# Performance work log

Measured on AMD Instinct MI355X. Metric: run time of the kernel, lower is better.

## Reference

```python
import jax, jax.numpy as jnp
import numpy as np

HID = 8
PRED_LEN = 12
SCALE = 4.4


def lstm_cell(x, h, c, Wih, Whh, bih, bhh):
    # torch.nn.LSTMCell gate order: i, f, g, o
    gates = x @ Wih.T + h @ Whh.T + (bih + bhh)  # (B, 4*HID)
    i, f, g, o = jnp.split(gates, 4, axis=-1)
    i = jax.nn.sigmoid(i)
    f = jax.nn.sigmoid(f)
    g = jnp.tanh(g)
    o = jax.nn.sigmoid(o)
    c_new = f * c + i * g
    h_new = o * jnp.tanh(c_new)
    return h_new, c_new


def setup_inputs() -> dict:
    key = jax.random.key(0)
    ks = jax.random.split(key, 12)
    B = 1048576
    obs_traj = jax.random.normal(ks[0], (8, B, 2), dtype=jnp.float32)
    h0 = jax.random.normal(ks[1], (B, HID), dtype=jnp.float32)
    c0 = jax.random.normal(ks[2], (B, HID), dtype=jnp.float32)
    s = 0.1
    Wih_t = jax.random.normal(ks[3], (4 * HID, 2), dtype=jnp.float32) * s
    Whh_t = jax.random.normal(ks[4], (4 * HID, HID), dtype=jnp.float32) * s
    bih_t = jax.random.normal(ks[5], (4 * HID,), dtype=jnp.float32) * s
    bhh_t = jax.random.normal(ks[6], (4 * HID,), dtype=jnp.float32) * s
    Wih_p = jax.random.normal(ks[7], (4 * HID, 2), dtype=jnp.float32) * s
    Whh_p = jax.random.normal(ks[8], (4 * HID, HID), dtype=jnp.float32) * s
    bih_p = jax.random.normal(ks[9], (4 * HID,), dtype=jnp.float32) * s
    bhh_p = jax.random.normal(ks[10], (4 * HID,), dtype=jnp.float32) * s
    Wp = jax.random.normal(ks[11], (2, HID), dtype=jnp.float32) * s
    bp = jnp.zeros((2,), dtype=jnp.float32)
    return {"obs_traj": obs_traj, "h0": h0, "c0": c0,
            "Wih_t": Wih_t, "Whh_t": Whh_t, "bih_t": bih_t, "bhh_t": bhh_t,
            "Wih_p": Wih_p, "Whh_p": Whh_p, "bih_p": bih_p, "bhh_p": bhh_p,
            "Wp": Wp, "bp": bp}


def reference(obs_traj, h0, c0, Wih_t, Whh_t, bih_t, bhh_t,
              Wih_p, Whh_p, bih_p, bhh_p, Wp, bp):
    B = obs_traj.shape[1]

    # --- encoder: scan over obs_len steps ---
    def enc_step(carry, x_t):
        h, c = carry
        x = jax.nn.relu(x_t)  # F.relu(input_t)
        h, c = lstm_cell(x, h, c, Wih_t, Whh_t, bih_t, bhh_t)
        return (h, c), None

    (h_enc, _), _ = jax.lax.scan(enc_step, (h0, c0), obs_traj)

    h_dec = h_enc
    c_dec = jnp.zeros_like(h_enc)
    out0 = jnp.zeros((B, 2), dtype=obs_traj.dtype)

    def dec_step(carry, _):
        h, c, out = carry
        x = jax.lax.stop_gradient(out)  # output.detach()
        h, c = lstm_cell(x, h, c, Wih_p, Whh_p, bih_p, bhh_p)
        out = jnp.tanh(h @ Wp.T + bp) * SCALE
        return (h, c, out), out

    _, pred_traj = jax.lax.scan(dec_step, (h_dec, c_dec, out0), None, length=PRED_LEN)
    return pred_traj  # (PRED_LEN, B, 2)
```

## Files before the change

kernel.cpp:

```cpp
#include <hip/hip_runtime.h>

#define HID 8
#define OBS_LEN 8
#define PRED_LEN 12
#define SCALE 4.4f
#define BLOCK 256
#define ELEMS_PER_BLOCK 128

typedef __attribute__((ext_vector_type(8)))  _Float16 half8;
typedef __attribute__((ext_vector_type(16))) float    f32x16;

#define LOG2E 1.44269504f

struct AB { half8 hi, lo; };
struct H2 { _Float16 hi, lo; };

__device__ __forceinline__ H2 split1(float v) {
    H2 r;
    r.hi = (_Float16)v;
    r.lo = (_Float16)(v - (float)r.hi);
    return r;
}

__device__ __forceinline__ void inv_pair(float a, float b, float& ia, float& ib) {
    const float r = __builtin_amdgcn_rcpf(a * b);
    ia = r * b;
    ib = r * a;
}

__device__ __forceinline__ AB build_A(int m, int half,
    const float* __restrict__ Wih, const float* __restrict__ Whh,
    const float* __restrict__ bih, const float* __restrict__ bhh)
{
    float w[8];
    if (half == 0) {
        w[0] = Wih[m * 2 + 0];
        w[1] = Wih[m * 2 + 1];
        w[2] = Whh[m * 8 + 0];
        w[3] = Whh[m * 8 + 1];
        w[4] = Whh[m * 8 + 2];
        w[5] = Whh[m * 8 + 3];
        w[6] = bih[m] + bhh[m];
        w[7] = 0.0f;
    } else {
        w[0] = 0.0f;
        w[1] = 0.0f;
        w[2] = Whh[m * 8 + 4];
        w[3] = Whh[m * 8 + 5];
        w[4] = Whh[m * 8 + 6];
        w[5] = Whh[m * 8 + 7];
        w[6] = 0.0f;
        w[7] = 0.0f;
    }
    AB r;
#pragma unroll
    for (int i = 0; i < 8; ++i) {
        const H2 s = split1(w[i]);
        r.hi[i] = s.hi;
        r.lo[i] = s.lo;
    }
    return r;
}

__device__ __forceinline__ AB build_B(float x0, float x1, const float h[4]) {
    AB r;
    const float v[6] = { x0, x1, h[0], h[1], h[2], h[3] };
#pragma unroll
    for (int i = 0; i < 6; ++i) {
        const H2 s = split1(v[i]);
        r.hi[i] = s.hi;
        r.lo[i] = s.lo;
    }
    r.hi[6] = (_Float16)1.0f; r.lo[6] = (_Float16)0.0f;
    r.hi[7] = (_Float16)0.0f; r.lo[7] = (_Float16)0.0f;
    return r;
}

__device__ __forceinline__ void lstm_pointwise(const f32x16& acc, float c[4], float h[4]) {
    float num1[4], den1[4], uo[4];
#pragma unroll
    for (int j = 0; j < 4; ++j) {
        const float ai = acc[j], af = acc[4 + j], ag = acc[8 + j], ao = acc[12 + j];
        const float ei = __builtin_amdgcn_exp2f(ai * -LOG2E);
        const float ef = __builtin_amdgcn_exp2f(af * -LOG2E);
        const float eg = __builtin_amdgcn_exp2f(ag * (-2.0f * LOG2E));
        const float eo = __builtin_amdgcn_exp2f(ao * -LOG2E);
        const float ui = 1.0f + ei, uf = 1.0f + ef, vg = 1.0f + eg;
        const float tg = 1.0f - eg;
        const float uiv = ui * vg;
        num1[j] = fmaf(tg, uf, c[j] * uiv);
        den1[j] = uf * uiv;
        uo[j] = 1.0f + eo;
    }
    float inv1[4];
    inv_pair(den1[0], den1[1], inv1[0], inv1[1]);
    inv_pair(den1[2], den1[3], inv1[2], inv1[3]);

    float den2[4], tc[4];
#pragma unroll
    for (int j = 0; j < 4; ++j) {
        const float cn = num1[j] * inv1[j];
        c[j] = cn;
        const float s = fminf(cn * (-2.0f * LOG2E), 43.0f);
        const float ec = __builtin_amdgcn_exp2f(s);
        den2[j] = uo[j] * (1.0f + ec);
        tc[j] = 1.0f - ec;
    }
    float inv2[4];
    inv_pair(den2[0], den2[1], inv2[0], inv2[1]);
    inv_pair(den2[2], den2[3], inv2[2], inv2[3]);
#pragma unroll
    for (int j = 0; j < 4; ++j) h[j] = tc[j] * inv2[j];
}

__device__ __forceinline__ void lstm_mfma_step(const AB& A, const AB& B,
                                               float c[4], float h[4]) {
    f32x16 acc = {};
    acc = __builtin_amdgcn_mfma_f32_32x32x16_f16(A.hi, B.hi, acc, 0, 0, 0);
    acc = __builtin_amdgcn_mfma_f32_32x32x16_f16(A.hi, B.lo, acc, 0, 0, 0);
    acc = __builtin_amdgcn_mfma_f32_32x32x16_f16(A.lo, B.hi, acc, 0, 0, 0);
    lstm_pointwise(acc, c, h);
}

__global__ __launch_bounds__(BLOCK) void MYLSTM_88201448390683_kernel(
    const float* __restrict__ obs,
    const float* __restrict__ h0,
    const float* __restrict__ c0,
    const float* __restrict__ Wih_t, const float* __restrict__ Whh_t,
    const float* __restrict__ bih_t, const float* __restrict__ bhh_t,
    const float* __restrict__ Wih_p, const float* __restrict__ Whh_p,
    const float* __restrict__ bih_p, const float* __restrict__ bhh_p,
    const float* __restrict__ Wp,
    const float* __restrict__ bp,
    float* __restrict__ out,
    int B)
{
    const int lane = threadIdx.x & 63;
    const int wid  = threadIdx.x >> 6;
    const int e    = lane & 31;
    const int half = lane >> 5;

    int eg = blockIdx.x * ELEMS_PER_BLOCK + wid * 32 + e;
    const bool ok = eg < B;
    if (!ok) eg = 0;

    float h[4], c[4];
    {
        const float4 hv = *reinterpret_cast<const float4*>(h0 + (size_t)eg * HID + half * 4);
        const float4 cv = *reinterpret_cast<const float4*>(c0 + (size_t)eg * HID + half * 4);
        h[0] = hv.x; h[1] = hv.y; h[2] = hv.z; h[3] = hv.w;
        c[0] = cv.x; c[1] = cv.y; c[2] = cv.z; c[3] = cv.w;
    }

    {
        const AB Aenc = build_A(e, half, Wih_t, Whh_t, bih_t, bhh_t);
#pragma unroll 1
        for (int t = 0; t < OBS_LEN; ++t) {
            const float2 xv = *reinterpret_cast<const float2*>(obs + ((size_t)t * B + eg) * 2);
            const AB Bv = build_B(fmaxf(xv.x, 0.0f), fmaxf(xv.y, 0.0f), h);
            lstm_mfma_step(Aenc, Bv, c, h);
        }
    }

    const AB Adec = build_A(e, half, Wih_p, Whh_p, bih_p, bhh_p);
#pragma unroll
    for (int j = 0; j < 4; ++j) c[j] = 0.0f;

    float wa[4], wb[4];
#pragma unroll
    for (int j = 0; j < 4; ++j) {
        wa[j] = Wp[4 * half + j];
        wb[j] = Wp[HID + 4 * half + j];
    }
    const float bp0 = bp[0], bp1 = bp[1];

    float x0 = 0.0f, x1 = 0.0f;
#pragma unroll 1
    for (int t = 0; t < PRED_LEN; ++t) {
        const AB Bv = build_B(x0, x1, h);
        lstm_mfma_step(Adec, Bv, c, h);
        float a0 = wa[0] * h[0] + wa[1] * h[1] + wa[2] * h[2] + wa[3] * h[3];
        float a1 = wb[0] * h[0] + wb[1] * h[1] + wb[2] * h[2] + wb[3] * h[3];
        a0 += __shfl_xor(a0, 32);
        a1 += __shfl_xor(a1, 32);
        a0 += bp0; a1 += bp1;
        const float e0 = __builtin_amdgcn_exp2f(a0 * (-2.0f * LOG2E));
        const float e1 = __builtin_amdgcn_exp2f(a1 * (-2.0f * LOG2E));
        float i0, i1;
        inv_pair(1.0f + e0, 1.0f + e1, i0, i1);
        x0 = (1.0f - e0) * i0 * SCALE;
        x1 = (1.0f - e1) * i1 * SCALE;
        if (!half && ok) {
            *reinterpret_cast<float2*>(out + ((size_t)t * B + eg) * 2) = make_float2(x0, x1);
        }
    }
}

extern "C" void kernel_launch(void* const* d_in, const int* in_sizes, int n_in,
                              void* d_out, int out_size, void* d_ws, size_t ws_size,
                              hipStream_t stream) {
    const float* obs   = (const float*)d_in[0];
    const float* h0    = (const float*)d_in[1];
    const float* c0    = (const float*)d_in[2];
    const float* Wih_t = (const float*)d_in[3];
    const float* Whh_t = (const float*)d_in[4];
    const float* bih_t = (const float*)d_in[5];
    const float* bhh_t = (const float*)d_in[6];
    const float* Wih_p = (const float*)d_in[7];
    const float* Whh_p = (const float*)d_in[8];
    const float* bih_p = (const float*)d_in[9];
    const float* bhh_p = (const float*)d_in[10];
    const float* Wp    = (const float*)d_in[11];
    const float* bp    = (const float*)d_in[12];
    float* out = (float*)d_out;

    const int B = in_sizes[1] / HID;
    const int grid = (B + ELEMS_PER_BLOCK - 1) / ELEMS_PER_BLOCK;

    hipLaunchKernelGGL(MYLSTM_88201448390683_kernel, dim3(grid), dim3(BLOCK), 0, stream,
                       obs, h0, c0,
                       Wih_t, Whh_t, bih_t, bhh_t,
                       Wih_p, Whh_p, bih_p, bhh_p,
                       Wp, bp, out, B);
}
```

Before: 367.1 us.

## Fold exp2 scaling into MFMA weights and vectorize LSTM pointwise math as packed float2

Pre-multiplies the gate weights and biases by -log2e (or -2·log2e for the g gate) so the MFMA accumulator feeds exp2 directly, removing per-element multiplies. Rewrites the pointwise math using 2-wide float vectors so the compiler can emit packed FP32 ops, uses cvt_pkrtz for the fp16 hi/lo splits, and merges the four reciprocals per step into a single rcp. Adds a clamp on the g-gate exponent and lowers the tanh(c) clamp. Risks: round-to-zero fp16 conversion, the fourfold product feeding one rcp could overflow or underflow, and the clamps may cause small accuracy differences.

```diff
diff --git a/kernel.cpp b/kernel.cpp
--- a/kernel.cpp
+++ b/kernel.cpp
@@ -7,116 +7,132 @@
 #define BLOCK 256
 #define ELEMS_PER_BLOCK 128
 
+#define LOG2E 1.44269504f
+#define ECLAMP 16.0f
+
 typedef __attribute__((ext_vector_type(8)))  _Float16 half8;
+typedef __attribute__((ext_vector_type(2)))  _Float16 half2v;
 typedef __attribute__((ext_vector_type(16))) float    f32x16;
-
-#define LOG2E 1.44269504f
-
+typedef __attribute__((ext_vector_type(2)))  float    v2f;
+
+union H8 { half8 v; half2v p[4]; };
 struct AB { half8 hi, lo; };
-struct H2 { _Float16 hi, lo; };
-
-__device__ __forceinline__ H2 split1(float v) {
-    H2 r;
-    r.hi = (_Float16)v;
-    r.lo = (_Float16)(v - (float)r.hi);
+
+__device__ __forceinline__ v2f splat(float v) { v2f r; r.x = v; r.y = v; return r; }
+
+__device__ __forceinline__ v2f exp2v(v2f a) {
+    v2f r;
+    r.x = __builtin_amdgcn_exp2f(a.x);
+    r.y = __builtin_amdgcn_exp2f(a.y);
     return r;
 }
 
-__device__ __forceinline__ void inv_pair(float a, float b, float& ia, float& ib) {
-    const float r = __builtin_amdgcn_rcpf(a * b);
-    ia = r * b;
-    ib = r * a;
-}
-
-__device__ __forceinline__ AB build_A(int m, int half,
+__device__ __forceinline__ half2v pkrtz(float a, float b) {
+    return __builtin_bit_cast(half2v, __builtin_amdgcn_cvt_pkrtz(a, b));
+}
+
+__device__ __forceinline__ void split_pair(float a, float b, half2v& hi, half2v& lo) {
+    hi = pkrtz(a, b);
+    lo = pkrtz(a - (float)hi.x, b - (float)hi.y);
+}
+
+__device__ __forceinline__ void quad_inv(const v2f d[2], v2f inv[2]) {
+    const v2f p2 = d[0] * d[1];
+    const float r = __builtin_amdgcn_rcpf(p2.x * p2.y);
+    const v2f t = splat(r) * p2;
+    v2f ts; ts.x = t.y; ts.y = t.x;
+    inv[0] = ts * d[1];
+    inv[1] = ts * d[0];
+}
+
+__device__ __forceinline__ AB build_A(int m, int half_,
     const float* __restrict__ Wih, const float* __restrict__ Whh,
     const float* __restrict__ bih, const float* __restrict__ bhh)
 {
+    const float k = ((m >> 3) == 2) ? (-2.0f * LOG2E) : (-LOG2E);
     float w[8];
-    if (half == 0) {
-        w[0] = Wih[m * 2 + 0];
-        w[1] = Wih[m * 2 + 1];
-        w[2] = Whh[m * 8 + 0];
-        w[3] = Whh[m * 8 + 1];
-        w[4] = Whh[m * 8 + 2];
-        w[5] = Whh[m * 8 + 3];
-        w[6] = bih[m] + bhh[m];
+    if (half_ == 0) {
+        w[0] = Wih[m * 2 + 0] * k;
+        w[1] = Wih[m * 2 + 1] * k;
+        w[2] = Whh[m * 8 + 0] * k;
+        w[3] = Whh[m * 8 + 1] * k;
+        w[4] = Whh[m * 8 + 2] * k;
+        w[5] = Whh[m * 8 + 3] * k;
+        w[6] = (bih[m] + bhh[m]) * k;
         w[7] = 0.0f;
     } else {
         w[0] = 0.0f;
         w[1] = 0.0f;
-        w[2] = Whh[m * 8 + 4];
-        w[3] = Whh[m * 8 + 5];
-        w[4] = Whh[m * 8 + 6];
-        w[5] = Whh[m * 8 + 7];
+        w[2] = Whh[m * 8 + 4] * k;
+        w[3] = Whh[m * 8 + 5] * k;
+        w[4] = Whh[m * 8 + 6] * k;
+        w[5] = Whh[m * 8 + 7] * k;
         w[6] = 0.0f;
         w[7] = 0.0f;
     }
-    AB r;
+    H8 hi, lo;
 #pragma unroll
-    for (int i = 0; i < 8; ++i) {
-        const H2 s = split1(w[i]);
-        r.hi[i] = s.hi;
-        r.lo[i] = s.lo;
-    }
+    for (int i = 0; i < 4; ++i) split_pair(w[2 * i], w[2 * i + 1], hi.p[i], lo.p[i]);
+    AB r; r.hi = hi.v; r.lo = lo.v;
     return r;
 }
 
-__device__ __forceinline__ AB build_B(float x0, float x1, const float h[4]) {
-    AB r;
-    const float v[6] = { x0, x1, h[0], h[1], h[2], h[3] };
+__device__ __forceinline__ AB build_B(float x0, float x1, const v2f h[2]) {
+    H8 hi, lo;
+    split_pair(x0, x1, hi.p[0], lo.p[0]);
+    split_pair(h[0].x, h[0].y, hi.p[1], lo.p[1]);
+    split_pair(h[1].x, h[1].y, hi.p[2], lo.p[2]);
+    const half2v one0 = {(_Float16)1.0f, (_Float16)0.0f};
+    const half2v zz   = {(_Float16)0.0f, (_Float16)0.0f};
+    hi.p[3] = one0;
+    lo.p[3] = zz;
+    AB r; r.hi = hi.v; r.lo = lo.v;
+    return r;
+}
+
+__device__ __forceinline__ void lstm_pointwise(const f32x16& acc, v2f c[2], v2f h[2]) {
+    v2f num1[2], den1[2], uo[2];
 #pragma unroll
-    for (int i = 0; i < 6; ++i) {
-        const H2 s = split1(v[i]);
-        r.hi[i] = s.hi;
-        r.lo[i] = s.lo;
-    }
-    r.hi[6] = (_Float16)1.0f; r.lo[6] = (_Float16)0.0f;
-    r.hi[7] = (_Float16)0.0f; r.lo[7] = (_Float16)0.0f;
-    return r;
-}
-
-__device__ __forceinline__ void lstm_pointwise(const f32x16& acc, float c[4], float h[4]) {
-    float num1[4], den1[4], uo[4];
+    for (int p = 0; p < 2; ++p) {
+        v2f ai, af, agr, ao;
+        ai.x  = acc[2 * p + 0];  ai.y  = acc[2 * p + 1];
+        af.x  = acc[4 + 2 * p];  af.y  = acc[5 + 2 * p];
+        agr.x = acc[8 + 2 * p];  agr.y = acc[9 + 2 * p];
+        ao.x  = acc[12 + 2 * p]; ao.y  = acc[13 + 2 * p];
+        const v2f ag = __builtin_elementwise_min(agr, splat(ECLAMP));
+        const v2f ei = exp2v(ai);
+        const v2f ef = exp2v(af);
+        const v2f eg = exp2v(ag);
+        const v2f eo = exp2v(ao);
+        const v2f ui = 1.0f + ei, uf = 1.0f + ef, vg = 1.0f + eg;
+        const v2f tg = 1.0f - eg;
+        const v2f uiv = ui * vg;
+        num1[p] = tg * uf + c[p] * uiv;
+        den1[p] = uf * uiv;
+        uo[p] = 1.0f + eo;
+    }
+    v2f inv1[2];
+    quad_inv(den1, inv1);
+
+    v2f den2[2], tc[2];
 #pragma unroll
-    for (int j = 0; j < 4; ++j) {
-        const float ai = acc[j], af = acc[4 + j], ag = acc[8 + j], ao = acc[12 + j];
-        const float ei = __builtin_amdgcn_exp2f(ai * -LOG2E);
-        const float ef = __builtin_amdgcn_exp2f(af * -LOG2E);
-        const float eg = __builtin_amdgcn_exp2f(ag * (-2.0f * LOG2E));
-        const float eo = __builtin_amdgcn_exp2f(ao * -LOG2E);
-        const float ui = 1.0f + ei, uf = 1.0f + ef, vg = 1.0f + eg;
-        const float tg = 1.0f - eg;
-        const float uiv = ui * vg;
-        num1[j] = fmaf(tg, uf, c[j] * uiv);
-        den1[j] = uf * uiv;
-        uo[j] = 1.0f + eo;
-    }
-    float inv1[4];
-    inv_pair(den1[0], den1[1], inv1[0], inv1[1]);
-    inv_pair(den1[2], den1[3], inv1[2], inv1[3]);
-
-    float den2[4], tc[4];
-#pragma unroll
-    for (int j = 0; j < 4; ++j) {
-        const float cn = num1[j] * inv1[j];
-        c[j] = cn;
-        const float s = fminf(cn * (-2.0f * LOG2E), 43.0f);
-        const float ec = __builtin_amdgcn_exp2f(s);
-        den2[j] = uo[j] * (1.0f + ec);
-        tc[j] = 1.0f - ec;
-    }
-    float inv2[4];
-    inv_pair(den2[0], den2[1], inv2[0], inv2[1]);
-    inv_pair(den2[2], den2[3], inv2[2], inv2[3]);
-#pragma unroll
-    for (int j = 0; j < 4; ++j) h[j] = tc[j] * inv2[j];
-}
-
-__device__ __forceinline__ void lstm_mfma_step(const AB& A, const AB& B,
-                                               float c[4], float h[4]) {
-    f32x16 acc = {};
-    acc = __builtin_amdgcn_mfma_f32_32x32x16_f16(A.hi, B.hi, acc, 0, 0, 0);
+    for (int p = 0; p < 2; ++p) {
+        const v2f cn = num1[p] * inv1[p];
+        c[p] = cn;
+        const v2f s = __builtin_elementwise_min(cn * (-2.0f * LOG2E), splat(ECLAMP));
+        const v2f ec = exp2v(s);
+        den2[p] = uo[p] * (1.0f + ec);
+        tc[p] = 1.0f - ec;
+    }
+    v2f inv2[2];
+    quad_inv(den2, inv2);
+    h[0] = tc[0] * inv2[0];
+    h[1] = tc[1] * inv2[1];
+}
+
+__device__ __forceinline__ void lstm_mfma_step(const AB& A, const AB& B, const f32x16& Z,
+                                               v2f c[2], v2f h[2]) {
+    f32x16 acc = __builtin_amdgcn_mfma_f32_32x32x16_f16(A.hi, B.hi, Z, 0, 0, 0);
     acc = __builtin_amdgcn_mfma_f32_32x32x16_f16(A.hi, B.lo, acc, 0, 0, 0);
     acc = __builtin_amdgcn_mfma_f32_32x32x16_f16(A.lo, B.hi, acc, 0, 0, 0);
     lstm_pointwise(acc, c, h);
@@ -144,52 +160,56 @@
     const bool ok = eg < B;
     if (!ok) eg = 0;
 
-    float h[4], c[4];
+    const f32x16 kZero = {};
+
+    v2f h[2], c[2];
     {
         const float4 hv = *reinterpret_cast<const float4*>(h0 + (size_t)eg * HID + half * 4);
         const float4 cv = *reinterpret_cast<const float4*>(c0 + (size_t)eg * HID + half * 4);
-        h[0] = hv.x; h[1] = hv.y; h[2] = hv.z; h[3] = hv.w;
-        c[0] = cv.x; c[1] = cv.y; c[2] = cv.z; c[3] = cv.w;
+        h[0].x = hv.x; h[0].y = hv.y; h[1].x = hv.z; h[1].y = hv.w;
+        c[0].x = cv.x; c[0].y = cv.y; c[1].x = cv.z; c[1].y = cv.w;
     }
 
     {
         const AB Aenc = build_A(e, half, Wih_t, Whh_t, bih_t, bhh_t);
 #pragma unroll 1
         for (int t = 0; t < OBS_LEN; ++t) {
-            const float2 xv = *reinterpret_cast<const float2*>(obs + ((size_t)t * B + eg) * 2);
-            const AB Bv = build_B(fmaxf(xv.x, 0.0f), fmaxf(xv.y, 0.0f), h);
-            lstm_mfma_step(Aenc, Bv, c, h);
+            const v2f xv = *reinterpret_cast<const v2f*>(obs + ((size_t)t * B + eg) * 2);
+            const v2f xr = __builtin_elementwise_max(xv, splat(0.0f));
+            const AB Bv = build_B(xr.x, xr.y, h);
+            lstm_mfma_step(Aenc, Bv, kZero, c, h);
         }
     }
 
     const AB Adec = build_A(e, half, Wih_p, Whh_p, bih_p, bhh_p);
-#pragma unroll
-    for (int j = 0; j < 4; ++j) c[j] = 0.0f;
-
-    float wa[4], wb[4];
-#pragma unroll
-    for (int j = 0; j < 4; ++j) {
-        wa[j] = Wp[4 * half + j];
-        wb[j] = Wp[HID + 4 * half + j];
-    }
+    c[0] = splat(0.0f);
+    c[1] = splat(0.0f);
+
+    v2f wa[2], wb[2];
+    wa[0].x = Wp[4 * half + 0];       wa[0].y = Wp[4 * half + 1];
+    wa[1].x = Wp[4 * half + 2];       wa[1].y = Wp[4 * half + 3];
+    wb[0].x = Wp[HID + 4 * half + 0]; wb[0].y = Wp[HID + 4 * half + 1];
+    wb[1].x = Wp[HID + 4 * half + 2]; wb[1].y = Wp[HID + 4 * half + 3];
     const float bp0 = bp[0], bp1 = bp[1];
 
     float x0 = 0.0f, x1 = 0.0f;
 #pragma unroll 1
     for (int t = 0; t < PRED_LEN; ++t) {
         const AB Bv = build_B(x0, x1, h);
-        lstm_mfma_step(Adec, Bv, c, h);
-        float a0 = wa[0] * h[0] + wa[1] * h[1] + wa[2] * h[2] + wa[3] * h[3];
-        float a1 = wb[0] * h[0] + wb[1] * h[1] + wb[2] * h[2] + wb[3] * h[3];
+        lstm_mfma_step(Adec, Bv, kZero, c, h);
+        const v2f q0 = wa[0] * h[0] + wa[1] * h[1];
+        const v2f q1 = wb[0] * h[0] + wb[1] * h[1];
+        float a0 = q0.x + q0.y;
+        float a1 = q1.x + q1.y;
         a0 += __shfl_xor(a0, 32);
         a1 += __shfl_xor(a1, 32);
-        a0 += bp0; a1 += bp1;
-        const float e0 = __builtin_amdgcn_exp2f(a0 * (-2.0f * LOG2E));
-        const float e1 = __builtin_amdgcn_exp2f(a1 * (-2.0f * LOG2E));
-        float i0, i1;
-        inv_pair(1.0f + e0, 1.0f + e1, i0, i1);
-        x0 = (1.0f - e0) * i0 * SCALE;
-        x1 = (1.0f - e1) * i1 * SCALE;
+        v2f av; av.x = a0 + bp0; av.y = a1 + bp1;
+        const v2f ev = exp2v(av * (-2.0f * LOG2E));
+        const v2f den = 1.0f + ev;
+        const float r = __builtin_amdgcn_rcpf(den.x * den.y);
+        v2f invv; invv.x = r * den.y; invv.y = r * den.x;
+        const v2f xv = (1.0f - ev) * invv * SCALE;
+        x0 = xv.x; x1 = xv.y;
         if (!half && ok) {
             *reinterpret_cast<float2*>(out + ((size_t)t * B + eg) * 2) = make_float2(x0, x1);
         }
```

Measured after the change: 346.4 us. 1.06x faster.
